# Kernel optimization log

Measured on AMD Instinct MI355X. Metric: run time of the kernel, lower is better.

## Reference

```python
import jax, jax.numpy as jnp
import numpy as np
from jax import lax

B, L, H, D = 4, 2048, 16, 64
STATE_DIM = 64


def setup_inputs() -> dict:
    key = jax.random.key(0)
    ks = jax.random.split(key, 9)
    return {
        "k": jax.random.normal(ks[0], (B, L, H, D), jnp.float32),
        "v": jax.random.normal(ks[1], (B, L, H, D), jnp.float32),
        "dt": jax.random.uniform(ks[2], (B, L, H, D), jnp.float32),
        "B_vec": jax.random.normal(ks[3], (B, L, STATE_DIM), jnp.float32),
        "C_vec": jax.random.normal(ks[4], (B, L, STATE_DIM), jnp.float32),
        "r": jax.random.normal(ks[5], (B, L, H, D), jnp.float32),
        "g": jax.random.normal(ks[6], (B, L, H, D), jnp.float32),
        "base_decay": jax.random.uniform(ks[7], (H, D), jnp.float32),
        "time_first": jax.random.normal(ks[8], (H, D), jnp.float32),
    }


def reference(k, v, dt, B_vec, C_vec, r, g, base_decay, time_first):
    # k, v, dt, r, g: [B, L, H, D]; B_vec, C_vec: [B, L, N]; base_decay, time_first: [H, D]
    Bz, Lz, Hz, Dz = k.shape
    state0 = jnp.zeros((Bz, Hz, Dz, Dz), dtype=k.dtype)

    def step(state, inp):
        kt, vt, dtt, Bt = inp  # kt/vt/dtt: [B,H,D]; Bt: [B,N]
        decay = jnp.exp(-base_decay * dtt)              # [B,H,D]
        state = decay[..., None] * state                # decay keys of state [B,H,D,D]
        kv_outer = jnp.einsum('bhk,bhv->bhkv', kt, vt)  # [B,H,D,D]
        B_scale = jnp.mean(Bt, axis=-1)[:, None, None, None]  # [B,1,1,1]
        state = state + B_scale * kv_outer
        wkv = jnp.einsum('bhkv,bhk->bhv', state, kt)    # [B,H,D]
        wkv = wkv + time_first * kt * vt                # bonus for current token
        return state, wkv

    # time-major for scan
    xs = (jnp.moveaxis(k, 1, 0), jnp.moveaxis(v, 1, 0),
          jnp.moveaxis(dt, 1, 0), jnp.moveaxis(B_vec, 1, 0))
    final_state, wkv_seq = lax.scan(step, state0, xs)
    wkv_seq = jnp.moveaxis(wkv_seq, 0, 1)               # [B,L,H,D]
    output = r * wkv_seq * g
    return output, final_state
```

## Files before the change

### kernel.cpp

```cpp
#include <hip/hip_runtime.h>


#define B_SZ 4
#define L_SZ 2048
#define H_SZ 16
#define D_SZ 64
#define T_CH 64
#define C_CH (L_SZ / T_CH)
#define BH (B_SZ * H_SZ)
#define STRIDE_T (H_SZ * D_SZ)

typedef short short8 __attribute__((ext_vector_type(8)));
typedef float f32x4 __attribute__((ext_vector_type(4)));

#define SWZ(row, col) (((row) << 6) + ((col) ^ (((row) & 7) << 3)))

__device__ __forceinline__ ushort f2bf(float x) {
    unsigned u = __float_as_uint(x);
    u += 0x7FFFu + ((u >> 16) & 1u);
    return (ushort)(u >> 16);
}
__device__ __forceinline__ float bf2f(ushort x) {
    return __uint_as_float(((unsigned)x) << 16);
}

__global__ __launch_bounds__(256) void bs_kernel(const float* __restrict__ Bvec,
                                                 float* __restrict__ Bs) {
    int wid = (blockIdx.x * 256 + threadIdx.x) >> 6;
    int lane = threadIdx.x & 63;
    if (wid >= B_SZ * L_SZ) return;
    float s = Bvec[wid * D_SZ + lane];
    #pragma unroll
    for (int m = 32; m >= 1; m >>= 1) s += __shfl_xor(s, m, 64);
    if (lane == 0) Bs[wid] = s * (1.0f / 64.0f);
}

__global__ __launch_bounds__(256, 4) void phase1_mfma(
    const float* __restrict__ kq, const float* __restrict__ vq,
    const float* __restrict__ dq, const float* __restrict__ Bs,
    const float* __restrict__ bd, float* __restrict__ P,
    ushort* __restrict__ Qbf)
{
    int c = blockIdx.x, bh = blockIdx.y;
    int b = bh >> 4, h = bh & 15;
    int tid = threadIdx.x;
    __shared__ __align__(16) ushort tKT[4096];
    __shared__ __align__(16) ushort tVT[4096];
    __shared__ float part[4][D_SZ];
    __shared__ float aTs[D_SZ];

    int t0 = c * T_CH;
    size_t base = ((size_t)(b * L_SZ + t0) * H_SZ + h) * D_SZ;
    int col = tid & 63, qq = tid >> 6;

    float dts[16], kin[16], vin[16];
    #pragma unroll
    for (int j = 0; j < 16; j++) {
        size_t off = base + (size_t)(qq * 16 + j) * STRIDE_T + col;
        dts[j] = dq[off];
        kin[j] = kq[off];
        vin[j] = vq[off];
    }
    float psum = 0.f;
    #pragma unroll
    for (int j = 0; j < 16; j++) psum += dts[j];
    part[qq][col] = psum;
    __syncthreads();

    float cs = 0.f;
    {
        float p0 = part[0][col], p1 = part[1][col], p2 = part[2][col];
        if (qq > 0) cs += p0;
        if (qq > 1) cs += p1;
        if (qq > 2) cs += p2;
    }
    float bdk = bd[h * D_SZ + col];
    short8 klo, khi, vlo, vhi;
    #pragma unroll
    for (int j = 0; j < 16; j++) {
        int t = qq * 16 + j;
        cs += dts[j];
        float bs = Bs[b * L_SZ + t0 + t];
        ushort kt = f2bf(bs * kin[j] * __expf(bdk * cs));
        ushort vt = f2bf(vin[j]);
        if (j < 8) { klo[j] = (short)kt; vlo[j] = (short)vt; }
        else       { khi[j - 8] = (short)kt; vhi[j - 8] = (short)vt; }
    }
    if (qq == 3) aTs[col] = __expf(-bdk * cs);
    *(short8*)&tKT[SWZ(col, qq * 16)]     = klo;
    *(short8*)&tKT[SWZ(col, qq * 16 + 8)] = khi;
    *(short8*)&tVT[SWZ(col, qq * 16)]     = vlo;
    *(short8*)&tVT[SWZ(col, qq * 16 + 8)] = vhi;
    __syncthreads();

    int lane = tid & 63, w = tid >> 6;
    int lg = lane >> 4, lr = lane & 15;
    f32x4 acc[4] = {};
    #pragma unroll
    for (int s = 0; s < 2; s++) {
        short8 a = *(const short8*)&tKT[SWZ(16 * w + lr, 32 * s + lg * 8)];
        #pragma unroll
        for (int j = 0; j < 4; j++) {
            short8 bv = *(const short8*)&tVT[SWZ(16 * j + lr, 32 * s + lg * 8)];
            acc[j] = __builtin_amdgcn_mfma_f32_16x16x32_bf16(a, bv, acc[j], 0, 0, 0);
        }
    }

    size_t qb = (size_t)(bh * C_CH + c) * (D_SZ * D_SZ);
    #pragma unroll
    for (int j = 0; j < 4; j++) {
        #pragma unroll
        for (int reg = 0; reg < 4; reg++) {
            int k = 16 * w + lg * 4 + reg;
            Qbf[qb + k * D_SZ + 16 * j + lr] = f2bf(aTs[k] * acc[j][reg]);
        }
    }
    if (tid < D_SZ)
        P[(size_t)(bh * C_CH + c) * D_SZ + tid] = aTs[tid];
}

__global__ __launch_bounds__(64) void phase2(const float* __restrict__ P,
                                             ushort* __restrict__ Qrw,
                                             float* __restrict__ out2) {
    int bh = blockIdx.x, kqi = blockIdx.y;
    int lane = threadIdx.x;
    float S[16];
    #pragma unroll
    for (int i = 0; i < 16; i++) S[i] = 0.f;

    size_t pb = (size_t)bh * C_CH * D_SZ + kqi * 16;
    size_t qb = ((size_t)bh * C_CH * D_SZ + kqi * 16) * D_SZ + lane;
    const size_t qstep = (size_t)D_SZ * D_SZ;

    float pc[16]; ushort qc[16];
    #pragma unroll
    for (int i = 0; i < 16; i++) {
        pc[i] = P[pb + i];
        qc[i] = Qrw[qb + (size_t)i * D_SZ];
    }
    for (int c = 0; c < C_CH; c++) {
        float pn[16] = {}; ushort qn[16] = {};
        if (c < C_CH - 1) {
            #pragma unroll
            for (int i = 0; i < 16; i++) {
                pn[i] = P[pb + (size_t)(c + 1) * D_SZ + i];
                qn[i] = Qrw[qb + (size_t)(c + 1) * qstep + (size_t)i * D_SZ];
            }
        }
        #pragma unroll
        for (int i = 0; i < 16; i++) {
            Qrw[qb + (size_t)c * qstep + (size_t)i * D_SZ] = f2bf(S[i]);
            S[i] = fmaf(pc[i], S[i], bf2f(qc[i]));
            pc[i] = pn[i]; qc[i] = qn[i];
        }
    }
    size_t ob = ((size_t)bh * D_SZ + kqi * 16) * D_SZ + lane;
    #pragma unroll
    for (int i = 0; i < 16; i++) out2[ob + (size_t)i * D_SZ] = S[i];
}

__global__ __launch_bounds__(256, 4) void phase3_mfma(
    const float* __restrict__ kq, const float* __restrict__ vq,
    const float* __restrict__ dq, const float* __restrict__ rq,
    const float* __restrict__ gq, const float* __restrict__ Bs,
    const float* __restrict__ bd, const float* __restrict__ tf,
    const ushort* __restrict__ Sb, float* __restrict__ out)
{
    int c = blockIdx.x, bh = blockIdx.y;
    int b = bh >> 4, h = bh & 15;
    int tid = threadIdx.x;
    __shared__ __align__(16) ushort SH[16384];
    ushort* tQ  = SH;
    ushort* tKG = SH + 4096;
    ushort* tS0 = SH + 8192;
    ushort* tVT = SH + 12288;
    float*  ACC = (float*)SH;
    __shared__ float part[4][D_SZ];

    int t0 = c * T_CH;
    size_t base = ((size_t)(b * L_SZ + t0) * H_SZ + h) * D_SZ;
    size_t sb = (size_t)(bh * C_CH + c) * (D_SZ * D_SZ);
    int col = tid & 63, qq = tid >> 6;

    float dts[16], kin[16], vin[16];
    ushort s0c[16];
    #pragma unroll
    for (int j = 0; j < 16; j++) {
        int t = qq * 16 + j;
        size_t off = base + (size_t)t * STRIDE_T + col;
        dts[j] = dq[off];
        kin[j] = kq[off];
        vin[j] = vq[off];
        s0c[j] = Sb[sb + (size_t)t * D_SZ + col];
    }
    float psum = 0.f;
    #pragma unroll
    for (int j = 0; j < 16; j++) psum += dts[j];
    part[qq][col] = psum;
    __syncthreads();

    float cs = 0.f;
    {
        float p0 = part[0][col], p1 = part[1][col], p2 = part[2][col];
        if (qq > 0) cs += p0;
        if (qq > 1) cs += p1;
        if (qq > 2) cs += p2;
    }
    float bdk = bd[h * D_SZ + col];
    short8 vlo, vhi, slo, shi;
    #pragma unroll
    for (int j = 0; j < 16; j++) {
        int t = qq * 16 + j;
        cs += dts[j];
        float bs = Bs[b * L_SZ + t0 + t];
        tQ[SWZ(t, col)]  = f2bf(kin[j] * __expf(-bdk * cs));
        tKG[SWZ(t, col)] = f2bf(bs * kin[j] * __expf(bdk * cs));
        ushort vt = f2bf(vin[j]);
        if (j < 8) { vlo[j] = (short)vt; slo[j] = (short)s0c[j]; }
        else       { vhi[j - 8] = (short)vt; shi[j - 8] = (short)s0c[j]; }
    }
    *(short8*)&tVT[SWZ(col, qq * 16)]     = vlo;
    *(short8*)&tVT[SWZ(col, qq * 16 + 8)] = vhi;
    *(short8*)&tS0[SWZ(col, qq * 16)]     = slo;
    *(short8*)&tS0[SWZ(col, qq * 16 + 8)] = shi;
    __syncthreads();

    int lane = tid & 63, w = tid >> 6;
    int lg = lane >> 4, lr = lane & 15;

    f32x4 gacc[4] = {};
    f32x4 acc[4] = {};
    #pragma unroll
    for (int s = 0; s < 2; s++) {
        short8 a = *(const short8*)&tQ[SWZ(16 * w + lr, 32 * s + lg * 8)];
        #pragma unroll
        for (int j = 0; j < 4; j++) {
            short8 bk = *(const short8*)&tKG[SWZ(16 * j + lr, 32 * s + lg * 8)];
            gacc[j] = __builtin_amdgcn_mfma_f32_16x16x32_bf16(a, bk, gacc[j], 0, 0, 0);
            short8 b0 = *(const short8*)&tS0[SWZ(16 * j + lr, 32 * s + lg * 8)];
            acc[j] = __builtin_amdgcn_mfma_f32_16x16x32_bf16(a, b0, acc[j], 0, 0, 0);
        }
    }
    __syncthreads();

    #pragma unroll
    for (int j = 0; j < 4; j++) {
        #pragma unroll
        for (int reg = 0; reg < 4; reg++) {
            int t = 16 * w + lg * 4 + reg;
            int tau = 16 * j + lr;
            tKG[SWZ(t, tau)] = (tau <= t) ? f2bf(gacc[j][reg]) : (ushort)0;
        }
    }
    __syncthreads();

    #pragma unroll
    for (int s = 0; s < 2; s++) {
        short8 a = *(const short8*)&tKG[SWZ(16 * w + lr, 32 * s + lg * 8)];
        #pragma unroll
        for (int j = 0; j < 4; j++) {
            short8 bv = *(const short8*)&tVT[SWZ(16 * j + lr, 32 * s + lg * 8)];
            acc[j] = __builtin_amdgcn_mfma_f32_16x16x32_bf16(a, bv, acc[j], 0, 0, 0);
        }
    }
    __syncthreads();

    #pragma unroll
    for (int j = 0; j < 4; j++) {
        #pragma unroll
        for (int reg = 0; reg < 4; reg++) {
            int t = 16 * w + lg * 4 + reg;
            int v = 16 * j + lr;
            ACC[t * D_SZ + (v ^ (((t >> 2) & 1) << 4))] = acc[j][reg];
        }
    }
    __syncthreads();

    float tfv = tf[h * D_SZ + col];
    #pragma unroll
    for (int j = 0; j < 16; j++) {
        int t = qq * 16 + j;
        size_t off = base + (size_t)t * STRIDE_T + col;
        float a = ACC[t * D_SZ + (col ^ (((t >> 2) & 1) << 4))];
        out[off] = rq[off] * (a + tfv * kin[j] * vin[j]) * gq[off];
    }
}

extern "C" void kernel_launch(void* const* d_in, const int* in_sizes, int n_in,
                              void* d_out, int out_size, void* d_ws, size_t ws_size,
                              hipStream_t stream) {
    const float* k    = (const float*)d_in[0];
    const float* v    = (const float*)d_in[1];
    const float* dt   = (const float*)d_in[2];
    const float* Bvec = (const float*)d_in[3];
    const float* r    = (const float*)d_in[5];
    const float* g    = (const float*)d_in[6];
    const float* bd   = (const float*)d_in[7];
    const float* tf   = (const float*)d_in[8];

    float* out  = (float*)d_out;
    float* out2 = out + (size_t)B_SZ * L_SZ * H_SZ * D_SZ;

    float* Bs  = (float*)d_ws;
    float* P   = Bs + B_SZ * L_SZ;
    ushort* Qb = (ushort*)(P + (size_t)BH * C_CH * D_SZ);

    bs_kernel<<<dim3(B_SZ * L_SZ / 4), 256, 0, stream>>>(Bvec, Bs);
    phase1_mfma<<<dim3(C_CH, BH), 256, 0, stream>>>(k, v, dt, Bs, bd, P, Qb);
    phase2<<<dim3(BH, 4), 64, 0, stream>>>(P, Qb, out2);
    phase3_mfma<<<dim3(C_CH, BH), 256, 0, stream>>>(k, v, dt, r, g, Bs, bd, tf, Qb, out);
}
```

Baseline: 82.13 us.

## Process two chunks per block with register prefetch of next chunk

Each block in phase1 and phase3 now handles two consecutive chunks, halving the grid. Global loads for the second chunk are issued before the MFMA work on the first chunk so memory latency overlaps compute. Phase3 also loads r and g early and precomputes the bonus term. The cost is higher register pressure, with phase3 launch bounds lowered to 3 blocks per SM, and fewer blocks to fill the GPU.

```diff
diff --git a/kernel.cpp b/kernel.cpp
--- a/kernel.cpp
+++ b/kernel.cpp
@@ -23,6 +23,9 @@
 __device__ __forceinline__ float bf2f(ushort x) {
     return __uint_as_float(((unsigned)x) << 16);
 }
+
+struct CRegs3 { float dts[16], kin[16], vin[16]; ushort s0[16]; };
+struct CRegs1 { float dts[16], kin[16], vin[16]; };
 
 __global__ __launch_bounds__(256) void bs_kernel(const float* __restrict__ Bvec,
                                                  float* __restrict__ Bs) {
@@ -41,7 +44,7 @@
     const float* __restrict__ bd, float* __restrict__ P,
     ushort* __restrict__ Qbf)
 {
-    int c = blockIdx.x, bh = blockIdx.y;
+    int cx = blockIdx.x, bh = blockIdx.y;
     int b = bh >> 4, h = bh & 15;
     int tid = threadIdx.x;
     __shared__ __align__(16) ushort tKT[4096];
@@ -49,74 +52,83 @@
     __shared__ float part[4][D_SZ];
     __shared__ float aTs[D_SZ];
 
-    int t0 = c * T_CH;
-    size_t base = ((size_t)(b * L_SZ + t0) * H_SZ + h) * D_SZ;
     int col = tid & 63, qq = tid >> 6;
-
-    float dts[16], kin[16], vin[16];
-    #pragma unroll
-    for (int j = 0; j < 16; j++) {
-        size_t off = base + (size_t)(qq * 16 + j) * STRIDE_T + col;
-        dts[j] = dq[off];
-        kin[j] = kq[off];
-        vin[j] = vq[off];
-    }
-    float psum = 0.f;
-    #pragma unroll
-    for (int j = 0; j < 16; j++) psum += dts[j];
-    part[qq][col] = psum;
-    __syncthreads();
-
-    float cs = 0.f;
-    {
-        float p0 = part[0][col], p1 = part[1][col], p2 = part[2][col];
-        if (qq > 0) cs += p0;
-        if (qq > 1) cs += p1;
-        if (qq > 2) cs += p2;
-    }
+    int w = tid >> 6, lg = (tid & 63) >> 4, lr = tid & 15;
     float bdk = bd[h * D_SZ + col];
-    short8 klo, khi, vlo, vhi;
-    #pragma unroll
-    for (int j = 0; j < 16; j++) {
-        int t = qq * 16 + j;
-        cs += dts[j];
-        float bs = Bs[b * L_SZ + t0 + t];
-        ushort kt = f2bf(bs * kin[j] * __expf(bdk * cs));
-        ushort vt = f2bf(vin[j]);
-        if (j < 8) { klo[j] = (short)kt; vlo[j] = (short)vt; }
-        else       { khi[j - 8] = (short)kt; vhi[j - 8] = (short)vt; }
-    }
-    if (qq == 3) aTs[col] = __expf(-bdk * cs);
-    *(short8*)&tKT[SWZ(col, qq * 16)]     = klo;
-    *(short8*)&tKT[SWZ(col, qq * 16 + 8)] = khi;
-    *(short8*)&tVT[SWZ(col, qq * 16)]     = vlo;
-    *(short8*)&tVT[SWZ(col, qq * 16 + 8)] = vhi;
-    __syncthreads();
-
-    int lane = tid & 63, w = tid >> 6;
-    int lg = lane >> 4, lr = lane & 15;
-    f32x4 acc[4] = {};
-    #pragma unroll
-    for (int s = 0; s < 2; s++) {
-        short8 a = *(const short8*)&tKT[SWZ(16 * w + lr, 32 * s + lg * 8)];
+    size_t hb = (size_t)(b * L_SZ) * STRIDE_T + h * D_SZ + col;
+
+    auto issue = [&](CRegs1& R, int c) {
+        size_t base = hb + (size_t)(c * T_CH) * STRIDE_T;
+        #pragma unroll
+        for (int j = 0; j < 16; j++) {
+            size_t off = base + (size_t)(qq * 16 + j) * STRIDE_T;
+            R.dts[j] = dq[off];
+            R.kin[j] = kq[off];
+            R.vin[j] = vq[off];
+        }
+    };
+
+    auto run = [&](CRegs1& R, CRegs1& Rn, int c, int cn, bool pf) {
+        float psum = 0.f;
+        #pragma unroll
+        for (int j = 0; j < 16; j++) psum += R.dts[j];
+        part[qq][col] = psum;
+        __syncthreads();
+        float cs = 0.f;
+        {
+            float p0 = part[0][col], p1 = part[1][col], p2 = part[2][col];
+            if (qq > 0) cs += p0;
+            if (qq > 1) cs += p1;
+            if (qq > 2) cs += p2;
+        }
+        int bsb = b * L_SZ + c * T_CH;
+        short8 klo, khi, vlo, vhi;
+        #pragma unroll
+        for (int j = 0; j < 16; j++) {
+            int t = qq * 16 + j;
+            cs += R.dts[j];
+            float bs = Bs[bsb + t];
+            ushort kt = f2bf(bs * R.kin[j] * __expf(bdk * cs));
+            ushort vt = f2bf(R.vin[j]);
+            if (j < 8) { klo[j] = (short)kt; vlo[j] = (short)vt; }
+            else       { khi[j - 8] = (short)kt; vhi[j - 8] = (short)vt; }
+        }
+        if (qq == 3) aTs[col] = __expf(-bdk * cs);
+        *(short8*)&tKT[SWZ(col, qq * 16)]     = klo;
+        *(short8*)&tKT[SWZ(col, qq * 16 + 8)] = khi;
+        *(short8*)&tVT[SWZ(col, qq * 16)]     = vlo;
+        *(short8*)&tVT[SWZ(col, qq * 16 + 8)] = vhi;
+        if (pf) issue(Rn, cn);
+        __syncthreads();
+
+        f32x4 acc[4] = {};
+        #pragma unroll
+        for (int s = 0; s < 2; s++) {
+            short8 a = *(const short8*)&tKT[SWZ(16 * w + lr, 32 * s + lg * 8)];
+            #pragma unroll
+            for (int j = 0; j < 4; j++) {
+                short8 bv = *(const short8*)&tVT[SWZ(16 * j + lr, 32 * s + lg * 8)];
+                acc[j] = __builtin_amdgcn_mfma_f32_16x16x32_bf16(a, bv, acc[j], 0, 0, 0);
+            }
+        }
+        size_t qb = (size_t)(bh * C_CH + c) * (D_SZ * D_SZ);
         #pragma unroll
         for (int j = 0; j < 4; j++) {
-            short8 bv = *(const short8*)&tVT[SWZ(16 * j + lr, 32 * s + lg * 8)];
-            acc[j] = __builtin_amdgcn_mfma_f32_16x16x32_bf16(a, bv, acc[j], 0, 0, 0);
-        }
-    }
-
-    size_t qb = (size_t)(bh * C_CH + c) * (D_SZ * D_SZ);
-    #pragma unroll
-    for (int j = 0; j < 4; j++) {
-        #pragma unroll
-        for (int reg = 0; reg < 4; reg++) {
-            int k = 16 * w + lg * 4 + reg;
-            Qbf[qb + k * D_SZ + 16 * j + lr] = f2bf(aTs[k] * acc[j][reg]);
-        }
-    }
-    if (tid < D_SZ)
-        P[(size_t)(bh * C_CH + c) * D_SZ + tid] = aTs[tid];
+            #pragma unroll
+            for (int reg = 0; reg < 4; reg++) {
+                int k = 16 * w + lg * 4 + reg;
+                Qbf[qb + k * D_SZ + 16 * j + lr] = f2bf(aTs[k] * acc[j][reg]);
+            }
+        }
+        if (tid < D_SZ)
+            P[(size_t)(bh * C_CH + c) * D_SZ + tid] = aTs[tid];
+    };
+
+    CRegs1 RA, RB;
+    int c0 = 2 * cx, c1 = 2 * cx + 1;
+    issue(RA, c0);
+    run(RA, RB, c0, c1, true);
+    run(RB, RA, c1, c1, false);
 }
 
 __global__ __launch_bounds__(64) void phase2(const float* __restrict__ P,
@@ -159,14 +171,14 @@
     for (int i = 0; i < 16; i++) out2[ob + (size_t)i * D_SZ] = S[i];
 }
 
-__global__ __launch_bounds__(256, 4) void phase3_mfma(
+__global__ __launch_bounds__(256, 3) void phase3_mfma(
     const float* __restrict__ kq, const float* __restrict__ vq,
     const float* __restrict__ dq, const float* __restrict__ rq,
     const float* __restrict__ gq, const float* __restrict__ Bs,
     const float* __restrict__ bd, const float* __restrict__ tf,
     const ushort* __restrict__ Sb, float* __restrict__ out)
 {
-    int c = blockIdx.x, bh = blockIdx.y;
+    int cx = blockIdx.x, bh = blockIdx.y;
     int b = bh >> 4, h = bh & 15;
     int tid = threadIdx.x;
     __shared__ __align__(16) ushort SH[16384];
@@ -177,113 +189,131 @@
     float*  ACC = (float*)SH;
     __shared__ float part[4][D_SZ];
 
-    int t0 = c * T_CH;
-    size_t base = ((size_t)(b * L_SZ + t0) * H_SZ + h) * D_SZ;
-    size_t sb = (size_t)(bh * C_CH + c) * (D_SZ * D_SZ);
     int col = tid & 63, qq = tid >> 6;
-
-    float dts[16], kin[16], vin[16];
-    ushort s0c[16];
-    #pragma unroll
-    for (int j = 0; j < 16; j++) {
-        int t = qq * 16 + j;
-        size_t off = base + (size_t)t * STRIDE_T + col;
-        dts[j] = dq[off];
-        kin[j] = kq[off];
-        vin[j] = vq[off];
-        s0c[j] = Sb[sb + (size_t)t * D_SZ + col];
-    }
-    float psum = 0.f;
-    #pragma unroll
-    for (int j = 0; j < 16; j++) psum += dts[j];
-    part[qq][col] = psum;
-    __syncthreads();
-
-    float cs = 0.f;
-    {
-        float p0 = part[0][col], p1 = part[1][col], p2 = part[2][col];
-        if (qq > 0) cs += p0;
-        if (qq > 1) cs += p1;
-        if (qq > 2) cs += p2;
-    }
+    int w = tid >> 6, lg = (tid & 63) >> 4, lr = tid & 15;
     float bdk = bd[h * D_SZ + col];
-    short8 vlo, vhi, slo, shi;
-    #pragma unroll
-    for (int j = 0; j < 16; j++) {
-        int t = qq * 16 + j;
-        cs += dts[j];
-        float bs = Bs[b * L_SZ + t0 + t];
-        tQ[SWZ(t, col)]  = f2bf(kin[j] * __expf(-bdk * cs));
-        tKG[SWZ(t, col)] = f2bf(bs * kin[j] * __expf(bdk * cs));
-        ushort vt = f2bf(vin[j]);
-        if (j < 8) { vlo[j] = (short)vt; slo[j] = (short)s0c[j]; }
-        else       { vhi[j - 8] = (short)vt; shi[j - 8] = (short)s0c[j]; }
-    }
-    *(short8*)&tVT[SWZ(col, qq * 16)]     = vlo;
-    *(short8*)&tVT[SWZ(col, qq * 16 + 8)] = vhi;
-    *(short8*)&tS0[SWZ(col, qq * 16)]     = slo;
-    *(short8*)&tS0[SWZ(col, qq * 16 + 8)] = shi;
-    __syncthreads();
-
-    int lane = tid & 63, w = tid >> 6;
-    int lg = lane >> 4, lr = lane & 15;
-
-    f32x4 gacc[4] = {};
-    f32x4 acc[4] = {};
-    #pragma unroll
-    for (int s = 0; s < 2; s++) {
-        short8 a = *(const short8*)&tQ[SWZ(16 * w + lr, 32 * s + lg * 8)];
+    float tfv = tf[h * D_SZ + col];
+    size_t hb = (size_t)(b * L_SZ) * STRIDE_T + h * D_SZ + col;
+
+    auto issue = [&](CRegs3& R, int c) {
+        size_t base = hb + (size_t)(c * T_CH) * STRIDE_T;
+        size_t sb = (size_t)(bh * C_CH + c) * (D_SZ * D_SZ);
+        #pragma unroll
+        for (int j = 0; j < 16; j++) {
+            int t = qq * 16 + j;
+            size_t off = base + (size_t)t * STRIDE_T;
+            R.dts[j] = dq[off];
+            R.kin[j] = kq[off];
+            R.vin[j] = vq[off];
+            R.s0[j]  = Sb[sb + (size_t)t * D_SZ + col];
+        }
+    };
+
+    auto run = [&](CRegs3& R, CRegs3& Rn, int c, int cn, bool pf) {
+        size_t base = hb + (size_t)(c * T_CH) * STRIDE_T;
+        float psum = 0.f;
+        #pragma unroll
+        for (int j = 0; j < 16; j++) psum += R.dts[j];
+        part[qq][col] = psum;
+        __syncthreads();
+        float cs = 0.f;
+        {
+            float p0 = part[0][col], p1 = part[1][col], p2 = part[2][col];
+            if (qq > 0) cs += p0;
+            if (qq > 1) cs += p1;
+            if (qq > 2) cs += p2;
+        }
+        int bsb = b * L_SZ + c * T_CH;
+        float bon[16];
+        short8 vlo, vhi, slo, shi;
+        #pragma unroll
+        for (int j = 0; j < 16; j++) {
+            int t = qq * 16 + j;
+            cs += R.dts[j];
+            float bs = Bs[bsb + t];
+            tQ[SWZ(t, col)]  = f2bf(R.kin[j] * __expf(-bdk * cs));
+            tKG[SWZ(t, col)] = f2bf(bs * R.kin[j] * __expf(bdk * cs));
+            ushort vt = f2bf(R.vin[j]);
+            bon[j] = tfv * R.kin[j] * R.vin[j];
+            if (j < 8) { vlo[j] = (short)vt; slo[j] = (short)R.s0[j]; }
+            else       { vhi[j - 8] = (short)vt; shi[j - 8] = (short)R.s0[j]; }
+        }
+        *(short8*)&tVT[SWZ(col, qq * 16)]     = vlo;
+        *(short8*)&tVT[SWZ(col, qq * 16 + 8)] = vhi;
+        *(short8*)&tS0[SWZ(col, qq * 16)]     = slo;
+        *(short8*)&tS0[SWZ(col, qq * 16 + 8)] = shi;
+        float rin[16], gin[16];
+        #pragma unroll
+        for (int j = 0; j < 16; j++) {
+            size_t off = base + (size_t)(qq * 16 + j) * STRIDE_T;
+            rin[j] = rq[off];
+            gin[j] = gq[off];
+        }
+        if (pf) issue(Rn, cn);
+        __syncthreads();
+
+        f32x4 gacc[4] = {};
+        f32x4 acc[4] = {};
+        #pragma unroll
+        for (int s = 0; s < 2; s++) {
+            short8 a = *(const short8*)&tQ[SWZ(16 * w + lr, 32 * s + lg * 8)];
+            #pragma unroll
+            for (int j = 0; j < 4; j++) {
+                short8 bk = *(const short8*)&tKG[SWZ(16 * j + lr, 32 * s + lg * 8)];
+                gacc[j] = __builtin_amdgcn_mfma_f32_16x16x32_bf16(a, bk, gacc[j], 0, 0, 0);
+                short8 b0 = *(const short8*)&tS0[SWZ(16 * j + lr, 32 * s + lg * 8)];
+                acc[j] = __builtin_amdgcn_mfma_f32_16x16x32_bf16(a, b0, acc[j], 0, 0, 0);
+            }
+        }
+        __syncthreads();
+
         #pragma unroll
         for (int j = 0; j < 4; j++) {
-            short8 bk = *(const short8*)&tKG[SWZ(16 * j + lr, 32 * s + lg * 8)];
-            gacc[j] = __builtin_amdgcn_mfma_f32_16x16x32_bf16(a, bk, gacc[j], 0, 0, 0);
-            short8 b0 = *(const short8*)&tS0[SWZ(16 * j + lr, 32 * s + lg * 8)];
-            acc[j] = __builtin_amdgcn_mfma_f32_16x16x32_bf16(a, b0, acc[j], 0, 0, 0);
-        }
-    }
-    __syncthreads();
-
-    #pragma unroll
-    for (int j = 0; j < 4; j++) {
-        #pragma unroll
-        for (int reg = 0; reg < 4; reg++) {
-            int t = 16 * w + lg * 4 + reg;
-            int tau = 16 * j + lr;
-            tKG[SWZ(t, tau)] = (tau <= t) ? f2bf(gacc[j][reg]) : (ushort)0;
-        }
-    }
-    __syncthreads();
-
-    #pragma unroll
-    for (int s = 0; s < 2; s++) {
-        short8 a = *(const short8*)&tKG[SWZ(16 * w + lr, 32 * s + lg * 8)];
+            #pragma unroll
+            for (int reg = 0; reg < 4; reg++) {
+                int t = 16 * w + lg * 4 + reg;
+                int tau = 16 * j + lr;
+                tKG[SWZ(t, tau)] = (tau <= t) ? f2bf(gacc[j][reg]) : (ushort)0;
+            }
+        }
+        __syncthreads();
+
+        #pragma unroll
+        for (int s = 0; s < 2; s++) {
+            short8 a = *(const short8*)&tKG[SWZ(16 * w + lr, 32 * s + lg * 8)];
+            #pragma unroll
+            for (int j = 0; j < 4; j++) {
+                short8 bv = *(const short8*)&tVT[SWZ(16 * j + lr, 32 * s + lg * 8)];
+                acc[j] = __builtin_amdgcn_mfma_f32_16x16x32_bf16(a, bv, acc[j], 0, 0, 0);
+            }
+        }
+        __syncthreads();
+
         #pragma unroll
         for (int j = 0; j < 4; j++) {
-            short8 bv = *(const short8*)&tVT[SWZ(16 * j + lr, 32 * s + lg * 8)];
-            acc[j] = __builtin_amdgcn_mfma_f32_16x16x32_bf16(a, bv, acc[j], 0, 0, 0);
-        }
-    }
-    __syncthreads();
-
-    #pragma unroll
-    for (int j = 0; j < 4; j++) {
-        #pragma unroll
-        for (int reg = 0; reg < 4; reg++) {
-            int t = 16 * w + lg * 4 + reg;
-            int v = 16 * j + lr;
-            ACC[t * D_SZ + (v ^ (((t >> 2) & 1) << 4))] = acc[j][reg];
-        }
-    }
-    __syncthreads();
-
-    float tfv = tf[h * D_SZ + col];
-    #pragma unroll
-    for (int j = 0; j < 16; j++) {
-        int t = qq * 16 + j;
-        size_t off = base + (size_t)t * STRIDE_T + col;
-        float a = ACC[t * D_SZ + (col ^ (((t >> 2) & 1) << 4))];
-        out[off] = rq[off] * (a + tfv * kin[j] * vin[j]) * gq[off];
-    }
+            #pragma unroll
+            for (int reg = 0; reg < 4; reg++) {
+                int t = 16 * w + lg * 4 + reg;
+                int v = 16 * j + lr;
+                ACC[t * D_SZ + (v ^ (((t >> 2) & 1) << 4))] = acc[j][reg];
+            }
+        }
+        __syncthreads();
+
+        #pragma unroll
+        for (int j = 0; j < 16; j++) {
+            int t = qq * 16 + j;
+            size_t off = base + (size_t)t * STRIDE_T;
+            float a = ACC[t * D_SZ + (col ^ (((t >> 2) & 1) << 4))];
+            out[off] = rin[j] * (a + bon[j]) * gin[j];
+        }
+    };
+
+    CRegs3 RA, RB;
+    int c0 = 2 * cx, c1 = 2 * cx + 1;
+    issue(RA, c0);
+    run(RA, RB, c0, c1, true);
+    run(RB, RA, c1, c1, false);
 }
 
 extern "C" void kernel_launch(void* const* d_in, const int* in_sizes, int n_in,
@@ -306,7 +336,7 @@
     ushort* Qb = (ushort*)(P + (size_t)BH * C_CH * D_SZ);
 
     bs_kernel<<<dim3(B_SZ * L_SZ / 4), 256, 0, stream>>>(Bvec, Bs);
-    phase1_mfma<<<dim3(C_CH, BH), 256, 0, stream>>>(k, v, dt, Bs, bd, P, Qb);
+    phase1_mfma<<<dim3(C_CH / 2, BH), 256, 0, stream>>>(k, v, dt, Bs, bd, P, Qb);
     phase2<<<dim3(BH, 4), 64, 0, stream>>>(P, Qb, out2);
-    phase3_mfma<<<dim3(C_CH, BH), 256, 0, stream>>>(k, v, dt, r, g, Bs, bd, tf, Qb, out);
-}
+    phase3_mfma<<<dim3(C_CH / 2, BH), 256, 0, stream>>>(k, v, dt, r, g, Bs, bd, tf, Qb, out);
+}
```

Measured after the change: 204.5 us. 2.49x slower.

## Process two chunks per phase3 block with software-prefetched loads

Applied to the files above, without the earlier changes.

Each phase3 block now handles two consecutive time chunks. It issues the second chunk's k/v/dt/state loads while the first chunk's MFMA work runs, and it loads r/g earlier, before the second matmul. This hides global memory latency and halves the grid size. The cost is more registers, so launch bounds drop to 3 blocks per SIMD set, and fewer blocks give less parallelism.

```diff
diff --git a/kernel.cpp b/kernel.cpp
--- a/kernel.cpp
+++ b/kernel.cpp
@@ -159,14 +159,125 @@
     for (int i = 0; i < 16; i++) out2[ob + (size_t)i * D_SZ] = S[i];
 }
 
-__global__ __launch_bounds__(256, 4) void phase3_mfma(
+#define P3_ISSUE(DTS, KIN, VIN, S0A, c)                                 \
+    {                                                                   \
+        size_t base_ = hb + (size_t)((c) * T_CH) * STRIDE_T;            \
+        size_t sb_ = (size_t)(bh * C_CH + (c)) * (D_SZ * D_SZ);         \
+        _Pragma("unroll")                                               \
+        for (int j = 0; j < 16; j++) {                                  \
+            int t = qq * 16 + j;                                        \
+            size_t off = base_ + (size_t)t * STRIDE_T;                  \
+            DTS[j] = dq[off];                                           \
+            KIN[j] = kq[off];                                           \
+            VIN[j] = vq[off];                                           \
+            S0A[j] = Sb[sb_ + (size_t)t * D_SZ + col];                  \
+        }                                                               \
+    }
+
+#define P3_RUN(DTS, KIN, VIN, S0A, c, PREFETCH)                           \
+    {                                                                     \
+        size_t base_ = hb + (size_t)((c) * T_CH) * STRIDE_T;              \
+        float psum = 0.f;                                                 \
+        _Pragma("unroll")                                                 \
+        for (int j = 0; j < 16; j++) psum += DTS[j];                      \
+        part[qq][col] = psum;                                             \
+        __syncthreads();   \
+        float cs = 0.f;                                                   \
+        {                                                                 \
+            float p0 = part[0][col], p1 = part[1][col], p2 = part[2][col];\
+            if (qq > 0) cs += p0;                                         \
+            if (qq > 1) cs += p1;                                         \
+            if (qq > 2) cs += p2;                                         \
+        }                                                                 \
+        int bsb = b * L_SZ + (c) * T_CH;                                  \
+        float bon[16];                                                    \
+        short8 vlo, vhi, slo, shi;                                        \
+        _Pragma("unroll")                                                 \
+        for (int j = 0; j < 16; j++) {                                    \
+            int t = qq * 16 + j;                                          \
+            cs += DTS[j];                                                 \
+            float bs = Bs[bsb + t];                                       \
+            tQ[SWZ(t, col)]  = f2bf(KIN[j] * __expf(-bdk * cs));          \
+            tKG[SWZ(t, col)] = f2bf(bs * KIN[j] * __expf(bdk * cs));      \
+            ushort vt = f2bf(VIN[j]);                                     \
+            bon[j] = tfv * KIN[j] * VIN[j];                               \
+            if (j < 8) { vlo[j] = (short)vt; slo[j] = (short)S0A[j]; }    \
+            else       { vhi[j - 8] = (short)vt; shi[j - 8] = (short)S0A[j]; } \
+        }                                                                 \
+        *(short8*)&tVT[SWZ(col, qq * 16)]     = vlo;                      \
+        *(short8*)&tVT[SWZ(col, qq * 16 + 8)] = vhi;                      \
+        *(short8*)&tS0[SWZ(col, qq * 16)]     = slo;                      \
+        *(short8*)&tS0[SWZ(col, qq * 16 + 8)] = shi;                      \
+        PREFETCH                                                          \
+        __syncthreads();                                          \
+        f32x4 gacc[4] = {};                                               \
+        f32x4 acc[4] = {};                                                \
+        _Pragma("unroll")                                                 \
+        for (int s = 0; s < 2; s++) {                                     \
+            short8 a = *(const short8*)&tQ[SWZ(16 * w + lr, 32 * s + lg * 8)]; \
+            _Pragma("unroll")                                             \
+            for (int j = 0; j < 4; j++) {                                 \
+                short8 bk = *(const short8*)&tKG[SWZ(16 * j + lr, 32 * s + lg * 8)]; \
+                gacc[j] = __builtin_amdgcn_mfma_f32_16x16x32_bf16(a, bk, gacc[j], 0, 0, 0); \
+                short8 b0 = *(const short8*)&tS0[SWZ(16 * j + lr, 32 * s + lg * 8)]; \
+                acc[j] = __builtin_amdgcn_mfma_f32_16x16x32_bf16(a, b0, acc[j], 0, 0, 0); \
+            }                                                             \
+        }                                                                 \
+        __syncthreads();                                          \
+        _Pragma("unroll")                                                 \
+        for (int j = 0; j < 4; j++) {                                     \
+            _Pragma("unroll")                                             \
+            for (int reg = 0; reg < 4; reg++) {                           \
+                int t = 16 * w + lg * 4 + reg;                            \
+                int tau = 16 * j + lr;                                    \
+                tKG[SWZ(t, tau)] = (tau <= t) ? f2bf(gacc[j][reg]) : (ushort)0; \
+            }                                                             \
+        }                                                                 \
+        __syncthreads();                                          \
+        float rin[16], gin[16];                                           \
+        _Pragma("unroll")                                                 \
+        for (int j = 0; j < 16; j++) {                                    \
+            size_t off = base_ + (size_t)(qq * 16 + j) * STRIDE_T;        \
+            rin[j] = rq[off];                                             \
+            gin[j] = gq[off];                                             \
+        }                                                                 \
+        _Pragma("unroll")                                                 \
+        for (int s = 0; s < 2; s++) {                                     \
+            short8 a = *(const short8*)&tKG[SWZ(16 * w + lr, 32 * s + lg * 8)]; \
+            _Pragma("unroll")                                             \
+            for (int j = 0; j < 4; j++) {                                 \
+                short8 bv = *(const short8*)&tVT[SWZ(16 * j + lr, 32 * s + lg * 8)]; \
+                acc[j] = __builtin_amdgcn_mfma_f32_16x16x32_bf16(a, bv, acc[j], 0, 0, 0); \
+            }                                                             \
+        }                                                                 \
+        __syncthreads();                     \
+        _Pragma("unroll")                                                 \
+        for (int j = 0; j < 4; j++) {                                     \
+            _Pragma("unroll")                                             \
+            for (int reg = 0; reg < 4; reg++) {                           \
+                int t = 16 * w + lg * 4 + reg;                            \
+                int v = 16 * j + lr;                                      \
+                ACC[t * D_SZ + (v ^ (((t >> 2) & 1) << 4))] = acc[j][reg]; \
+            }                                                             \
+        }                                                                 \
+        __syncthreads();                                          \
+        _Pragma("unroll")                                                 \
+        for (int j = 0; j < 16; j++) {                                    \
+            int t = qq * 16 + j;                                          \
+            size_t off = base_ + (size_t)t * STRIDE_T;                    \
+            float a = ACC[t * D_SZ + (col ^ (((t >> 2) & 1) << 4))];      \
+            out[off] = rin[j] * (a + bon[j]) * gin[j];                    \
+        }                                                                 \
+    }
+
+__global__ __launch_bounds__(256, 3) void phase3_mfma(
     const float* __restrict__ kq, const float* __restrict__ vq,
     const float* __restrict__ dq, const float* __restrict__ rq,
     const float* __restrict__ gq, const float* __restrict__ Bs,
     const float* __restrict__ bd, const float* __restrict__ tf,
     const ushort* __restrict__ Sb, float* __restrict__ out)
 {
-    int c = blockIdx.x, bh = blockIdx.y;
+    int cx = blockIdx.x, bh = blockIdx.y;
     int b = bh >> 4, h = bh & 15;
     int tid = threadIdx.x;
     __shared__ __align__(16) ushort SH[16384];
@@ -177,113 +288,20 @@
     float*  ACC = (float*)SH;
     __shared__ float part[4][D_SZ];
 
-    int t0 = c * T_CH;
-    size_t base = ((size_t)(b * L_SZ + t0) * H_SZ + h) * D_SZ;
-    size_t sb = (size_t)(bh * C_CH + c) * (D_SZ * D_SZ);
     int col = tid & 63, qq = tid >> 6;
-
-    float dts[16], kin[16], vin[16];
-    ushort s0c[16];
-    #pragma unroll
-    for (int j = 0; j < 16; j++) {
-        int t = qq * 16 + j;
-        size_t off = base + (size_t)t * STRIDE_T + col;
-        dts[j] = dq[off];
-        kin[j] = kq[off];
-        vin[j] = vq[off];
-        s0c[j] = Sb[sb + (size_t)t * D_SZ + col];
-    }
-    float psum = 0.f;
-    #pragma unroll
-    for (int j = 0; j < 16; j++) psum += dts[j];
-    part[qq][col] = psum;
-    __syncthreads();
-
-    float cs = 0.f;
-    {
-        float p0 = part[0][col], p1 = part[1][col], p2 = part[2][col];
-        if (qq > 0) cs += p0;
-        if (qq > 1) cs += p1;
-        if (qq > 2) cs += p2;
-    }
+    int w = tid >> 6, lg = (tid & 63) >> 4, lr = tid & 15;
     float bdk = bd[h * D_SZ + col];
-    short8 vlo, vhi, slo, shi;
-    #pragma unroll
-    for (int j = 0; j < 16; j++) {
-        int t = qq * 16 + j;
-        cs += dts[j];
-        float bs = Bs[b * L_SZ + t0 + t];
-        tQ[SWZ(t, col)]  = f2bf(kin[j] * __expf(-bdk * cs));
-        tKG[SWZ(t, col)] = f2bf(bs * kin[j] * __expf(bdk * cs));
-        ushort vt = f2bf(vin[j]);
-        if (j < 8) { vlo[j] = (short)vt; slo[j] = (short)s0c[j]; }
-        else       { vhi[j - 8] = (short)vt; shi[j - 8] = (short)s0c[j]; }
-    }
-    *(short8*)&tVT[SWZ(col, qq * 16)]     = vlo;
-    *(short8*)&tVT[SWZ(col, qq * 16 + 8)] = vhi;
-    *(short8*)&tS0[SWZ(col, qq * 16)]     = slo;
-    *(short8*)&tS0[SWZ(col, qq * 16 + 8)] = shi;
-    __syncthreads();
-
-    int lane = tid & 63, w = tid >> 6;
-    int lg = lane >> 4, lr = lane & 15;
-
-    f32x4 gacc[4] = {};
-    f32x4 acc[4] = {};
-    #pragma unroll
-    for (int s = 0; s < 2; s++) {
-        short8 a = *(const short8*)&tQ[SWZ(16 * w + lr, 32 * s + lg * 8)];
-        #pragma unroll
-        for (int j = 0; j < 4; j++) {
-            short8 bk = *(const short8*)&tKG[SWZ(16 * j + lr, 32 * s + lg * 8)];
-            gacc[j] = __builtin_amdgcn_mfma_f32_16x16x32_bf16(a, bk, gacc[j], 0, 0, 0);
-            short8 b0 = *(const short8*)&tS0[SWZ(16 * j + lr, 32 * s + lg * 8)];
-            acc[j] = __builtin_amdgcn_mfma_f32_16x16x32_bf16(a, b0, acc[j], 0, 0, 0);
-        }
-    }
-    __syncthreads();
-
-    #pragma unroll
-    for (int j = 0; j < 4; j++) {
-        #pragma unroll
-        for (int reg = 0; reg < 4; reg++) {
-            int t = 16 * w + lg * 4 + reg;
-            int tau = 16 * j + lr;
-            tKG[SWZ(t, tau)] = (tau <= t) ? f2bf(gacc[j][reg]) : (ushort)0;
-        }
-    }
-    __syncthreads();
-
-    #pragma unroll
-    for (int s = 0; s < 2; s++) {
-        short8 a = *(const short8*)&tKG[SWZ(16 * w + lr, 32 * s + lg * 8)];
-        #pragma unroll
-        for (int j = 0; j < 4; j++) {
-            short8 bv = *(const short8*)&tVT[SWZ(16 * j + lr, 32 * s + lg * 8)];
-            acc[j] = __builtin_amdgcn_mfma_f32_16x16x32_bf16(a, bv, acc[j], 0, 0, 0);
-        }
-    }
-    __syncthreads();
-
-    #pragma unroll
-    for (int j = 0; j < 4; j++) {
-        #pragma unroll
-        for (int reg = 0; reg < 4; reg++) {
-            int t = 16 * w + lg * 4 + reg;
-            int v = 16 * j + lr;
-            ACC[t * D_SZ + (v ^ (((t >> 2) & 1) << 4))] = acc[j][reg];
-        }
-    }
-    __syncthreads();
-
     float tfv = tf[h * D_SZ + col];
-    #pragma unroll
-    for (int j = 0; j < 16; j++) {
-        int t = qq * 16 + j;
-        size_t off = base + (size_t)t * STRIDE_T + col;
-        float a = ACC[t * D_SZ + (col ^ (((t >> 2) & 1) << 4))];
-        out[off] = rq[off] * (a + tfv * kin[j] * vin[j]) * gq[off];
-    }
+    size_t hb = (size_t)(b * L_SZ) * STRIDE_T + h * D_SZ + col;
+
+    int c0 = 2 * cx, c1 = 2 * cx + 1;
+
+    float dtsA[16], kinA[16], vinA[16]; ushort s0A[16];
+    float dtsB[16], kinB[16], vinB[16]; ushort s0B[16];
+
+    P3_ISSUE(dtsA, kinA, vinA, s0A, c0)
+    P3_RUN(dtsA, kinA, vinA, s0A, c0, P3_ISSUE(dtsB, kinB, vinB, s0B, c1))
+    P3_RUN(dtsB, kinB, vinB, s0B, c1, {})
 }
 
 extern "C" void kernel_launch(void* const* d_in, const int* in_sizes, int n_in,
@@ -308,5 +326,5 @@
     bs_kernel<<<dim3(B_SZ * L_SZ / 4), 256, 0, stream>>>(Bvec, Bs);
     phase1_mfma<<<dim3(C_CH, BH), 256, 0, stream>>>(k, v, dt, Bs, bd, P, Qb);
     phase2<<<dim3(BH, 4), 64, 0, stream>>>(P, Qb, out2);
-    phase3_mfma<<<dim3(C_CH, BH), 256, 0, stream>>>(k, v, dt, r, g, Bs, bd, tf, Qb, out);
-}
+    phase3_mfma<<<dim3(C_CH / 2, BH), 256, 0, stream>>>(k, v, dt, r, g, Bs, bd, tf, Qb, out);
+}
```

After: 145.0 us. 1.77x slower.
